# Optimization experiments

Measured on AMD Instinct MI355X. Metric: run time of the kernel, lower is better.

The kernel has to match this reference:

```python
import jax, jax.numpy as jnp
import numpy as np

NS, NV = 64, 32            # scalar channels (0e), vector channels (1o)
DIM = NS + 3 * NV          # 160, irreps feature dim
LAT, HID, NT = 128, 256, 4
N_NODES, N_EDGES, N_ACT = 50000, 300000, 200000
SQ3 = np.float32(np.sqrt(3.0))


def _split(x):
    return x[..., :NS], x[..., NS:].reshape(x.shape[:-1] + (NV, 3))


def _merge(s, v):
    return jnp.concatenate([s, v.reshape(v.shape[:-2] + (NV * 3,))], -1)


def _sln(x, gs, bs, gv, eps=1e-5):
    # Separable equivariant layer norm: standard LN on scalars,
    # RMS-of-norms normalization on vector channels.
    s, v = _split(x)
    mu = jnp.mean(s, -1, keepdims=True)
    var = jnp.var(s, -1, keepdims=True)
    s = (s - mu) * jax.lax.rsqrt(var + eps) * gs + bs
    n2 = jnp.sum(v * v, -1)                                  # [*, NV]
    rms = jnp.sqrt(jnp.mean(n2, -1, keepdims=True) + eps)    # [*, 1]
    v = v / rms[..., None] * gv[:, None]
    return _merge(s, v)


def setup_inputs():
    key = jax.random.key(0)
    ks = iter(jax.random.split(key, 32))
    nx = lambda: next(ks)

    def w(shape):
        return jax.random.normal(nx(), shape, jnp.float32) / np.float32(np.sqrt(shape[0]))

    latents = jax.random.normal(nx(), (N_EDGES, LAT), jnp.float32)
    node_features = jax.random.normal(nx(), (N_NODES, DIM), jnp.float32)
    types = jax.random.randint(nx(), (N_NODES,), 0, NT)
    node_onehot = jax.nn.one_hot(types, NT, dtype=jnp.float32)
    edge_features = jax.random.normal(nx(), (N_ACT, DIM), jnp.float32)
    vec = jax.random.normal(nx(), (N_ACT, 3), jnp.float32)
    unit = vec / jnp.linalg.norm(vec, axis=-1, keepdims=True)
    edge_sh = jnp.concatenate([jnp.ones((N_ACT, 1), jnp.float32), SQ3 * unit], -1)
    edge_index = jax.random.randint(nx(), (2, N_EDGES), 0, N_NODES)
    cutoff_coeffs = jax.random.uniform(nx(), (N_EDGES,), jnp.float32)
    active_edges = jnp.arange(N_ACT)

    return dict(
        latents=latents, node_features=node_features, node_onehot=node_onehot,
        edge_features=edge_features, edge_sh=edge_sh, edge_index=edge_index,
        cutoff_coeffs=cutoff_coeffs, active_edges=active_edges,
        sln_n_gs=jnp.ones(NS), sln_n_bs=jnp.zeros(NS), sln_n_gv=jnp.ones(NV),
        sln_e_gs=jnp.ones(NS), sln_e_bs=jnp.zeros(NS), sln_e_gv=jnp.ones(NV),
        ln_lat_g=jnp.ones(LAT), ln_lat_b=jnp.zeros(LAT),
        Wa=w((3 * NS, NS + NV)), Wb=w((3 * NV, NS + NV)),
        Wc=w((3 * NS, NV)), Wd=w((3 * NV, NV)),
        Wp_s=w((NS, NS)), Wp_v=w((NV, NV)),
        W_edge=w((LAT, NS + NV)),
        W_lat1=w((LAT + (NS + NV) + 2 * NT, HID)), W_lat2=w((HID, LAT)),
        Wres_s=w((NS, NS)), Wres_v=w((NV, NV)),
    )


def reference(latents, node_features, node_onehot, edge_features, edge_sh,
              edge_index, cutoff_coeffs, active_edges,
              sln_n_gs, sln_n_bs, sln_n_gv, sln_e_gs, sln_e_bs, sln_e_gv,
              ln_lat_g, ln_lat_b, Wa, Wb, Wc, Wd, Wp_s, Wp_v,
              W_edge, W_lat1, W_lat2, Wres_s, Wres_v):
    idx_i = edge_index[0][active_edges]
    idx_j = edge_index[1][active_edges]

    nf = _sln(node_features, sln_n_gs, sln_n_bs, sln_n_gv)
    node_i, node_j = nf[idx_i], nf[idx_j]
    ef = _sln(edge_features, sln_e_gs, sln_e_bs, sln_e_gv)

    s_i, v_i = _split(node_i)
    s_e, v_e = _split(ef)
    s_j, v_j = _split(node_j)
    s_all = jnp.concatenate([s_i, s_e, s_j], -1)   # [Ea, 3*NS]
    v_all = jnp.concatenate([v_i, v_e, v_j], -2)   # [Ea, 3*NV, 3]

    sh0, sh1 = edge_sh[:, :1], edge_sh[:, 1:]
    # Fully connected tensor product, CG paths with l<=1 and 0e/1o parity:
    #   0e x 0e -> 0e ; 1o x 1o -> 0e (dot / sqrt3) ; 0e x 1o -> 1o ; 1o x 0e -> 1o
    o_s = (s_all * sh0) @ Wa + (jnp.einsum('evc,ec->ev', v_all, sh1) / SQ3) @ Wb  # [Ea, NS+NV]
    o_v = (jnp.einsum('ei,ec,io->eoc', s_all, sh1, Wc)
           + jnp.einsum('evc,e,vo->eoc', v_all, sh0[:, 0], Wd))                    # [Ea, NV, 3]

    # Gate nonlinearity: silu on scalars, sigmoid gates on vector channels
    m_s = jax.nn.silu(o_s[:, :NS])
    m_v = o_v * jax.nn.sigmoid(o_s[:, NS:])[:, :, None]

    # lin_post (equivariant linear)
    m_s = m_s @ Wp_s
    m_v = jnp.einsum('evc,vw->ewc', m_v, Wp_v)

    # per-edge elementwise weights from latents (E3ElementLinear)
    lat_a = latents[active_edges]
    ww = lat_a @ W_edge                            # [Ea, NS+NV]
    e_s = m_s * ww[:, :NS]
    e_v = m_v * ww[:, NS:, None]

    # latent update MLP
    mu = jnp.mean(lat_a, -1, keepdims=True)
    var = jnp.var(lat_a, -1, keepdims=True)
    lat_n = (lat_a - mu) * jax.lax.rsqrt(var + 1e-5) * ln_lat_g + ln_lat_b
    lat_in = jnp.concatenate([node_onehot[idx_i], lat_n, o_s, node_onehot[idx_j]], -1)
    new_lat = (jax.nn.silu(lat_in @ W_lat1) @ W_lat2) * cutoff_coeffs[active_edges][:, None]
    latents_out = latents.at[active_edges].set(new_lat)   # index_copy

    # residual equivariant linear on raw edge features
    r_s, r_v = _split(edge_features)
    edge_out = _merge(e_s + r_s @ Wres_s,
                      e_v + jnp.einsum('evc,vw->ewc', r_v, Wres_v))
    return edge_out, latents_out
```

## Files before the change

kernel.cpp:

```cpp
#include <hip/hip_runtime.h>
#include <stdint.h>

#define NSC 64
#define NVC 32
#define DIMF 160
#define LATD 128
#define HIDD 256
#define N_EDGES_K 300000
#define N_ACT_K 200000
#define NE_TILE 8

typedef unsigned short u16;

__device__ __forceinline__ float b2f(u16 x) {
    union { unsigned int u; float f; } v; v.u = ((unsigned int)x) << 16; return v.f;
}
__device__ __forceinline__ u16 f2b(float f) {
    union { unsigned int u; float f; } v; v.f = f;
    return (u16)((v.u + 0x7fffu + ((v.u >> 16) & 1u)) >> 16);
}

template<int F32>
__device__ __forceinline__ float ldx(const void* p, size_t i) {
    if (F32) return ((const float*)p)[i];
    return b2f(((const u16*)p)[i]);
}
template<int F32>
__device__ __forceinline__ void stx(void* p, size_t i, float v) {
    if (!(fabsf(v) < 1e30f)) v = 12345.0f;
    if (F32) ((float*)p)[i] = v;
    else     ((u16*)p)[i] = f2b(v);
}

__device__ __forceinline__ float wsum(float v) {
#pragma unroll
    for (int m = 32; m > 0; m >>= 1) v += __shfl_xor(v, m, 64);
    return v;
}
__device__ __forceinline__ float fsig(float x)  { return 1.f / (1.f + __expf(-x)); }
__device__ __forceinline__ float fsilu(float x) { return x / (1.f + __expf(-x)); }

template<int F32>
__device__ __forceinline__ void norm_row(const void* __restrict__ row, size_t off,
                                         const void* __restrict__ gs,
                                         const void* __restrict__ bs,
                                         const void* __restrict__ gv,
                                         float* ds, float* dvp, int vbase, int lane) {
    float s  = ldx<F32>(row, off + lane);
    float va = ldx<F32>(row, off + 64 + lane);
    float vb = (lane < 32) ? ldx<F32>(row, off + 128 + lane) : 0.f;
    float mu  = wsum(s) * (1.f / 64.f);
    float var = wsum(s * s) * (1.f / 64.f) - mu * mu;
    float n2  = wsum(va * va + vb * vb);
    float invs = rsqrtf(var + 1e-5f);
    float invv = rsqrtf(n2 * (1.f / 32.f) + 1e-5f);
    ds[lane] = (s - mu) * invs * ldx<F32>(gs, lane) + ldx<F32>(bs, lane);
    int v1 = lane / 3, c1 = lane - 3 * v1;
    dvp[c1 * 96 + vbase + v1] = va * invv * ldx<F32>(gv, v1);
    if (lane < 32) {
        int p = 64 + lane;
        int v2 = p / 3, c2 = p - 3 * v2;
        dvp[c2 * 96 + vbase + v2] = vb * invv * ldx<F32>(gv, v2);
    }
}

__global__ void detect_kernel(const u16* __restrict__ probe, int* __restrict__ flag) {
    __shared__ int cnt;
    if (threadIdx.x == 0) cnt = 0;
    __syncthreads();
    u16 x = probe[threadIdx.x];
    int e = (x >> 7) & 0xFF;
    int sane = ((x & 0x7FFF) == 0) || (e >= 96 && e <= 143);
    atomicAdd(&cnt, sane);
    __syncthreads();
    if (threadIdx.x == 0) *flag = (cnt >= 240) ? 0 : 1;
}

template<int F32>
__global__ void copy_lat_kernel(const int* __restrict__ flag,
                                const uint4* __restrict__ in, uint4* __restrict__ out, int n) {
    if (*flag != F32) return;
    int i = blockIdx.x * blockDim.x + threadIdx.x;
    if (i < n) out[i] = in[i];
}

template<int F32>
__global__ __launch_bounds__(256, 3)
void edge_kernel(const int* __restrict__ flag,
                 const void* __restrict__ latents,
                 const void* __restrict__ nodef,
                 const void* __restrict__ onehot,
                 const void* __restrict__ edgef,
                 const void* __restrict__ esh,
                 const int* __restrict__ eidx,
                 const void* __restrict__ cutc,
                 const int* __restrict__ act,
                 const void* __restrict__ n_gs, const void* __restrict__ n_bs, const void* __restrict__ n_gv,
                 const void* __restrict__ e_gs, const void* __restrict__ e_bs, const void* __restrict__ e_gv,
                 const void* __restrict__ lg, const void* __restrict__ lb,
                 const void* __restrict__ Wa, const void* __restrict__ Wb,
                 const void* __restrict__ Wc, const void* __restrict__ Wd,
                 const void* __restrict__ Wps, const void* __restrict__ Wpv,
                 const void* __restrict__ Wedge, const void* __restrict__ Wl1,
                 const void* __restrict__ Wl2, const void* __restrict__ Wrs,
                 const void* __restrict__ Wrv,
                 void* __restrict__ out_edge, void* __restrict__ out_lat)
{
    if (*flag != F32) return;

    __shared__ float arena[NE_TILE][288];
    __shared__ float vall[NE_TILE][288];
    __shared__ float osb [NE_TILE][96];
    __shared__ float latb[NE_TILE][128];
    __shared__ float latn[NE_TILE][128];
    __shared__ float wwb [NE_TILE][96];
    __shared__ float mspb[NE_TILE][64];
    __shared__ float mvpb[NE_TILE][96];
    __shared__ float msvb[NE_TILE][160];
    __shared__ float hidb[NE_TILE][256];
    __shared__ float shb [NE_TILE][4];
    __shared__ float ohib[NE_TILE][4];
    __shared__ float ohjb[NE_TILE][4];
    __shared__ float cutb[NE_TILE];
    __shared__ int   aib [NE_TILE];

    const int tid  = threadIdx.x;
    const int wid  = tid >> 6;
    const int lane = tid & 63;
    const int base = blockIdx.x * NE_TILE;

    for (int t = wid; t < NE_TILE; t += 4) {
        const int E = base + t;
        const int a = act[E];
        const int i = eidx[a];
        const int j = eidx[N_EDGES_K + a];
        norm_row<F32>(nodef, (size_t)i * DIMF, n_gs, n_bs, n_gv, &arena[t][0],   &vall[t][0], 0,  lane);
        norm_row<F32>(edgef, (size_t)E * DIMF, e_gs, e_bs, e_gv, &arena[t][64],  &vall[t][0], 32, lane);
        norm_row<F32>(nodef, (size_t)j * DIMF, n_gs, n_bs, n_gv, &arena[t][128], &vall[t][0], 64, lane);
        float x0 = ldx<F32>(latents, (size_t)a * LATD + lane);
        float x1 = ldx<F32>(latents, (size_t)a * LATD + 64 + lane);
        float mu  = wsum(x0 + x1) * (1.f / 128.f);
        float var = wsum(x0 * x0 + x1 * x1) * (1.f / 128.f) - mu * mu;
        float inv = rsqrtf(var + 1e-5f);
        latb[t][lane]      = x0;
        latb[t][64 + lane] = x1;
        latn[t][lane]      = (x0 - mu) * inv * ldx<F32>(lg, lane)      + ldx<F32>(lb, lane);
        latn[t][64 + lane] = (x1 - mu) * inv * ldx<F32>(lg, 64 + lane) + ldx<F32>(lb, 64 + lane);
        if (lane < 4) {
            shb [t][lane] = ldx<F32>(esh, (size_t)E * 4 + lane);
            ohib[t][lane] = ldx<F32>(onehot, (size_t)i * 4 + lane);
            ohjb[t][lane] = ldx<F32>(onehot, (size_t)j * 4 + lane);
        }
        if (lane == 0) { cutb[t] = ldx<F32>(cutc, a); aib[t] = a; }
    }
    __syncthreads();

    for (int idx = tid; idx < NE_TILE * 96; idx += 256) {
        int t = idx / 96, v = idx - 96 * t;
        arena[t][192 + v] = (vall[t][v] * shb[t][1] + vall[t][96 + v] * shb[t][2] +
                             vall[t][192 + v] * shb[t][3]) * 0.5773502691896258f;
    }
    {
        const int o = tid & 31, t = tid >> 5;
        float s0 = 0.f, s1 = 0.f, s2 = 0.f, s3 = 0.f;
#pragma unroll 2
        for (int k = 0; k < 192; k += 4) {
            float w0 = ldx<F32>(Wc, (size_t)(k + 0) * 32 + o);
            float w1 = ldx<F32>(Wc, (size_t)(k + 1) * 32 + o);
            float w2 = ldx<F32>(Wc, (size_t)(k + 2) * 32 + o);
            float w3 = ldx<F32>(Wc, (size_t)(k + 3) * 32 + o);
            float4 a = *(const float4*)&arena[t][k];
            s0 += w0 * a.x; s1 += w1 * a.y; s2 += w2 * a.z; s3 += w3 * a.w;
        }
        hidb[t][o] = (s0 + s1) + (s2 + s3);
        float a0 = 0.f, a1 = 0.f, a2 = 0.f;
#pragma unroll 2
        for (int v = 0; v < 96; v += 4) {
            float w0 = ldx<F32>(Wd, (size_t)(v + 0) * 32 + o);
            float w1 = ldx<F32>(Wd, (size_t)(v + 1) * 32 + o);
            float w2 = ldx<F32>(Wd, (size_t)(v + 2) * 32 + o);
            float w3 = ldx<F32>(Wd, (size_t)(v + 3) * 32 + o);
            float4 p0 = *(const float4*)&vall[t][v];
            float4 p1 = *(const float4*)&vall[t][96 + v];
            float4 p2 = *(const float4*)&vall[t][192 + v];
            a0 += w0 * p0.x + w1 * p0.y + w2 * p0.z + w3 * p0.w;
            a1 += w0 * p1.x + w1 * p1.y + w2 * p1.z + w3 * p1.w;
            a2 += w0 * p2.x + w1 * p2.y + w2 * p2.z + w3 * p2.w;
        }
        hidb[t][32 + o] = a0;
        hidb[t][64 + o] = a1;
        hidb[t][96 + o] = a2;
    }
    __syncthreads();

    {
        const int o = tid % 96, g = tid / 96;
        if (g < 2) {
            const int t0 = g * 4;
            float acc[4] = {0, 0, 0, 0};
#pragma unroll 2
            for (int k = 0; k < 192; k += 4) {
                float w0 = ldx<F32>(Wa, (size_t)(k + 0) * 96 + o);
                float w1 = ldx<F32>(Wa, (size_t)(k + 1) * 96 + o);
                float w2 = ldx<F32>(Wa, (size_t)(k + 2) * 96 + o);
                float w3 = ldx<F32>(Wa, (size_t)(k + 3) * 96 + o);
#pragma unroll
                for (int e = 0; e < 4; ++e) {
                    float4 a = *(const float4*)&arena[t0 + e][k];
                    acc[e] += w0 * a.x + w1 * a.y + w2 * a.z + w3 * a.w;
                }
            }
#pragma unroll
            for (int e = 0; e < 4; ++e) acc[e] *= shb[t0 + e][0];
#pragma unroll 2
            for (int k = 0; k < 96; k += 4) {
                float w0 = ldx<F32>(Wb, (size_t)(k + 0) * 96 + o);
                float w1 = ldx<F32>(Wb, (size_t)(k + 1) * 96 + o);
                float w2 = ldx<F32>(Wb, (size_t)(k + 2) * 96 + o);
                float w3 = ldx<F32>(Wb, (size_t)(k + 3) * 96 + o);
#pragma unroll
                for (int e = 0; e < 4; ++e) {
                    float4 a = *(const float4*)&arena[t0 + e][192 + k];
                    acc[e] += w0 * a.x + w1 * a.y + w2 * a.z + w3 * a.w;
                }
            }
#pragma unroll
            for (int e = 0; e < 4; ++e) osb[t0 + e][o] = acc[e];
        }
    }
    __syncthreads();

    for (int idx = tid; idx < NE_TILE * 96; idx += 256) {
        int t = idx / 96, r = idx - 96 * t, c = r >> 5, o = r & 31;
        mvpb[t][r] = (hidb[t][o] * shb[t][1 + c] + hidb[t][32 + r] * shb[t][0]) * fsig(osb[t][64 + o]);
    }
    for (int idx = tid; idx < NE_TILE * 64; idx += 256) {
        int t = idx >> 6, o = idx & 63;
        mspb[t][o] = fsilu(osb[t][o]);
    }
    for (int idx = tid; idx < NE_TILE * 232; idx += 256) {
        int t = idx / 232, k = idx - 232 * t;
        float v;
        if (k < 4)        v = ohib[t][k];
        else if (k < 132) v = latn[t][k - 4];
        else if (k < 228) v = osb[t][k - 132];
        else              v = ohjb[t][k - 228];
        arena[t][k] = v;
    }
    for (int idx = tid; idx < NE_TILE * 160; idx += 256) {
        int t = idx / 160, d = idx - 160 * t;
        float val = ldx<F32>(edgef, (size_t)(base + t) * DIMF + d);
        if (d < 64) vall[t][d] = val;
        else { int r = d - 64, v = r / 3, c = r - 3 * v; vall[t][64 + c * 32 + v] = val; }
    }
    __syncthreads();

    {
        const int o = tid & 63, g = tid >> 6;
        const int t0 = g * 2;
        float acc0 = 0.f, acc1 = 0.f;
#pragma unroll 2
        for (int k = 0; k < 64; k += 4) {
            float w0 = ldx<F32>(Wps, (size_t)(k + 0) * 64 + o);
            float w1 = ldx<F32>(Wps, (size_t)(k + 1) * 64 + o);
            float w2 = ldx<F32>(Wps, (size_t)(k + 2) * 64 + o);
            float w3 = ldx<F32>(Wps, (size_t)(k + 3) * 64 + o);
            float4 a = *(const float4*)&mspb[t0][k];
            float4 b = *(const float4*)&mspb[t0 + 1][k];
            acc0 += w0 * a.x + w1 * a.y + w2 * a.z + w3 * a.w;
            acc1 += w0 * b.x + w1 * b.y + w2 * b.z + w3 * b.w;
        }
        msvb[t0][o]     = acc0;
        msvb[t0 + 1][o] = acc1;
        const int o2 = tid & 31, t = tid >> 5;
        float a0 = 0.f, a1 = 0.f, a2 = 0.f;
#pragma unroll 2
        for (int v = 0; v < 32; v += 4) {
            float w0 = ldx<F32>(Wpv, (size_t)(v + 0) * 32 + o2);
            float w1 = ldx<F32>(Wpv, (size_t)(v + 1) * 32 + o2);
            float w2 = ldx<F32>(Wpv, (size_t)(v + 2) * 32 + o2);
            float w3 = ldx<F32>(Wpv, (size_t)(v + 3) * 32 + o2);
            float4 q0 = *(const float4*)&mvpb[t][v];
            float4 q1 = *(const float4*)&mvpb[t][32 + v];
            float4 q2 = *(const float4*)&mvpb[t][64 + v];
            a0 += w0 * q0.x + w1 * q0.y + w2 * q0.z + w3 * q0.w;
            a1 += w0 * q1.x + w1 * q1.y + w2 * q1.z + w3 * q1.w;
            a2 += w0 * q2.x + w1 * q2.y + w2 * q2.z + w3 * q2.w;
        }
        msvb[t][64 + o2]  = a0;
        msvb[t][96 + o2]  = a1;
        msvb[t][128 + o2] = a2;
    }
    {
        const int o = tid % 96, g = tid / 96;
        if (g < 2) {
            const int t0 = g * 4;
            float acc[4] = {0, 0, 0, 0};
#pragma unroll 2
            for (int k = 0; k < 128; k += 4) {
                float w0 = ldx<F32>(Wedge, (size_t)(k + 0) * 96 + o);
                float w1 = ldx<F32>(Wedge, (size_t)(k + 1) * 96 + o);
                float w2 = ldx<F32>(Wedge, (size_t)(k + 2) * 96 + o);
                float w3 = ldx<F32>(Wedge, (size_t)(k + 3) * 96 + o);
#pragma unroll
                for (int e = 0; e < 4; ++e) {
                    float4 a = *(const float4*)&latb[t0 + e][k];
                    acc[e] += w0 * a.x + w1 * a.y + w2 * a.z + w3 * a.w;
                }
            }
#pragma unroll
            for (int e = 0; e < 4; ++e) wwb[t0 + e][o] = acc[e];
        }
    }
    {
        const int o = tid;
        float acc[NE_TILE] = {0, 0, 0, 0, 0, 0, 0, 0};
#pragma unroll 2
        for (int k = 0; k < 232; k += 4) {
            float w0 = ldx<F32>(Wl1, (size_t)(k + 0) * 256 + o);
            float w1 = ldx<F32>(Wl1, (size_t)(k + 1) * 256 + o);
            float w2 = ldx<F32>(Wl1, (size_t)(k + 2) * 256 + o);
            float w3 = ldx<F32>(Wl1, (size_t)(k + 3) * 256 + o);
#pragma unroll
            for (int e = 0; e < NE_TILE; ++e) {
                float4 a = *(const float4*)&arena[e][k];
                acc[e] += w0 * a.x + w1 * a.y + w2 * a.z + w3 * a.w;
            }
        }
#pragma unroll
        for (int e = 0; e < NE_TILE; ++e) hidb[e][o] = fsilu(acc[e]);
    }
    __syncthreads();

    {
        const int o = tid & 127, g = tid >> 7;
        const int t0 = g * 4;
        float acc[4] = {0, 0, 0, 0};
#pragma unroll 2
        for (int k = 0; k < 256; k += 4) {
            float w0 = ldx<F32>(Wl2, (size_t)(k + 0) * 128 + o);
            float w1 = ldx<F32>(Wl2, (size_t)(k + 1) * 128 + o);
            float w2 = ldx<F32>(Wl2, (size_t)(k + 2) * 128 + o);
            float w3 = ldx<F32>(Wl2, (size_t)(k + 3) * 128 + o);
#pragma unroll
            for (int e = 0; e < 4; ++e) {
                float4 a = *(const float4*)&hidb[t0 + e][k];
                acc[e] += w0 * a.x + w1 * a.y + w2 * a.z + w3 * a.w;
            }
        }
#pragma unroll
        for (int e = 0; e < 4; ++e) {
            int t = t0 + e;
            stx<F32>(out_lat, (size_t)aib[t] * LATD + o, acc[e] * cutb[t]);
        }
    }
    {
        const int o = tid & 63, g = tid >> 6;
        const int t0 = g * 2;
        float acc0 = 0.f, acc1 = 0.f;
#pragma unroll 2
        for (int k = 0; k < 64; k += 4) {
            float w0 = ldx<F32>(Wrs, (size_t)(k + 0) * 64 + o);
            float w1 = ldx<F32>(Wrs, (size_t)(k + 1) * 64 + o);
            float w2 = ldx<F32>(Wrs, (size_t)(k + 2) * 64 + o);
            float w3 = ldx<F32>(Wrs, (size_t)(k + 3) * 64 + o);
            float4 a = *(const float4*)&vall[t0][k];
            float4 b = *(const float4*)&vall[t0 + 1][k];
            acc0 += w0 * a.x + w1 * a.y + w2 * a.z + w3 * a.w;
            acc1 += w0 * b.x + w1 * b.y + w2 * b.z + w3 * b.w;
        }
        stx<F32>(out_edge, (size_t)(base + t0)     * DIMF + o, msvb[t0][o]     * wwb[t0][o]     + acc0);
        stx<F32>(out_edge, (size_t)(base + t0 + 1) * DIMF + o, msvb[t0 + 1][o] * wwb[t0 + 1][o] + acc1);
        const int o2 = tid & 31, t = tid >> 5;
        float a0 = 0.f, a1 = 0.f, a2 = 0.f;
#pragma unroll 2
        for (int v = 0; v < 32; v += 4) {
            float w0 = ldx<F32>(Wrv, (size_t)(v + 0) * 32 + o2);
            float w1 = ldx<F32>(Wrv, (size_t)(v + 1) * 32 + o2);
            float w2 = ldx<F32>(Wrv, (size_t)(v + 2) * 32 + o2);
            float w3 = ldx<F32>(Wrv, (size_t)(v + 3) * 32 + o2);
            float4 q0 = *(const float4*)&vall[t][64 + v];
            float4 q1 = *(const float4*)&vall[t][96 + v];
            float4 q2 = *(const float4*)&vall[t][128 + v];
            a0 += w0 * q0.x + w1 * q0.y + w2 * q0.z + w3 * q0.w;
            a1 += w0 * q1.x + w1 * q1.y + w2 * q1.z + w3 * q1.w;
            a2 += w0 * q2.x + w1 * q2.y + w2 * q2.z + w3 * q2.w;
        }
        float wv = wwb[t][64 + o2];
        size_t eb = (size_t)(base + t) * DIMF + 64;
        stx<F32>(out_edge, eb + 3 * o2    , msvb[t][64 + o2]  * wv + a0);
        stx<F32>(out_edge, eb + 3 * o2 + 1, msvb[t][96 + o2]  * wv + a1);
        stx<F32>(out_edge, eb + 3 * o2 + 2, msvb[t][128 + o2] * wv + a2);
    }
}

extern "C" void kernel_launch(void* const* d_in, const int* in_sizes, int n_in,
                              void* d_out, int out_size, void* d_ws, size_t ws_size,
                              hipStream_t stream) {
    const void* latents = d_in[0];
    const void* nodef   = d_in[1];
    const void* onehot  = d_in[2];
    const void* edgef   = d_in[3];
    const void* esh     = d_in[4];
    const int*  eidx    = (const int*)d_in[5];
    const void* cutc    = d_in[6];
    const int*  act     = (const int*)d_in[7];

    int* flag = (int*)d_ws;
    detect_kernel<<<1, 256, 0, stream>>>((const u16*)d_in[1], flag);

    const size_t EDGE_ELEMS = (size_t)N_ACT_K * DIMF;
    void* out_lat_b = (void*)((u16*)d_out + EDGE_ELEMS);
    void* out_lat_f = (void*)((float*)d_out + EDGE_ELEMS);

    copy_lat_kernel<0><<<(N_EDGES_K * LATD / 8) / 256, 256, 0, stream>>>(
        flag, (const uint4*)latents, (uint4*)out_lat_b, N_EDGES_K * LATD / 8);
    copy_lat_kernel<1><<<(N_EDGES_K * LATD / 4) / 256, 256, 0, stream>>>(
        flag, (const uint4*)latents, (uint4*)out_lat_f, N_EDGES_K * LATD / 4);

    edge_kernel<0><<<N_ACT_K / NE_TILE, 256, 0, stream>>>(
        flag, latents, nodef, onehot, edgef, esh, eidx, cutc, act,
        d_in[8], d_in[9], d_in[10], d_in[11], d_in[12], d_in[13], d_in[14], d_in[15],
        d_in[16], d_in[17], d_in[18], d_in[19], d_in[20], d_in[21], d_in[22], d_in[23],
        d_in[24], d_in[25], d_in[26],
        d_out, out_lat_b);
    edge_kernel<1><<<N_ACT_K / NE_TILE, 256, 0, stream>>>(
        flag, latents, nodef, onehot, edgef, esh, eidx, cutc, act,
        d_in[8], d_in[9], d_in[10], d_in[11], d_in[12], d_in[13], d_in[14], d_in[15],
        d_in[16], d_in[17], d_in[18], d_in[19], d_in[20], d_in[21], d_in[22], d_in[23],
        d_in[24], d_in[25], d_in[26],
        d_out, out_lat_f);
}
```

Baseline: 2.636 ms.

## Pre-convert weights to fp32 workspace and shrink shared memory for higher occupancy

Adds a conv kernel that copies all weight matrices and LN params into an fp32 workspace, so the edge kernel reads fp32 weights with no per-load bf16 conversion. Shared buffers are consolidated (hidb, latn, osb/wwb removed or aliased), the lat-LN is computed on the fly, and the residual reads edge features straight from global memory instead of restaging them. Together with launch_bounds raised to 4 blocks per CU, this targets occupancy and latency hiding. Costs are an extra launch, doubled weight bytes in bf16 mode, and uncoalesced global reads in the residual loop.

```diff
diff --git a/kernel.cpp b/kernel.cpp
--- a/kernel.cpp
+++ b/kernel.cpp
@@ -84,8 +84,33 @@
     if (i < n) out[i] = in[i];
 }
 
+#define NSEG 13
+__device__ __constant__ const int g_seg_sz[NSEG]  = {18432,9216,6144,3072,4096,1024,12288,59392,32768,4096,1024,128,128};
+__device__ __constant__ const int g_seg_off[NSEG] = {0,18432,27648,33792,36864,40960,41984,54272,113664,146432,150528,151552,151680};
+#define WS_FLOATS 151808
+
 template<int F32>
-__global__ __launch_bounds__(256, 3)
+__global__ void conv_kernel(const int* __restrict__ flag, float* __restrict__ dst,
+                            const void* p0, const void* p1, const void* p2, const void* p3,
+                            const void* p4, const void* p5, const void* p6, const void* p7,
+                            const void* p8, const void* p9, const void* p10, const void* p11,
+                            const void* p12) {
+    if (*flag != F32) return;
+    int s = blockIdx.y;
+    int i = blockIdx.x * blockDim.x + threadIdx.x;
+    const void* p;
+    switch (s) {
+        case 0: p = p0; break;  case 1: p = p1; break;  case 2: p = p2; break;
+        case 3: p = p3; break;  case 4: p = p4; break;  case 5: p = p5; break;
+        case 6: p = p6; break;  case 7: p = p7; break;  case 8: p = p8; break;
+        case 9: p = p9; break;  case 10: p = p10; break; case 11: p = p11; break;
+        default: p = p12; break;
+    }
+    if (i < g_seg_sz[s]) dst[g_seg_off[s] + i] = ldx<F32>(p, i);
+}
+
+template<int F32, int WCONV>
+__global__ __launch_bounds__(256, 4)
 void edge_kernel(const int* __restrict__ flag,
                  const void* __restrict__ latents,
                  const void* __restrict__ nodef,
@@ -97,7 +122,7 @@
                  const int* __restrict__ act,
                  const void* __restrict__ n_gs, const void* __restrict__ n_bs, const void* __restrict__ n_gv,
                  const void* __restrict__ e_gs, const void* __restrict__ e_bs, const void* __restrict__ e_gv,
-                 const void* __restrict__ lg, const void* __restrict__ lb,
+                 const void* __restrict__ LG, const void* __restrict__ LB,
                  const void* __restrict__ Wa, const void* __restrict__ Wb,
                  const void* __restrict__ Wc, const void* __restrict__ Wd,
                  const void* __restrict__ Wps, const void* __restrict__ Wpv,
@@ -107,21 +132,21 @@
                  void* __restrict__ out_edge, void* __restrict__ out_lat)
 {
     if (*flag != F32) return;
+    constexpr int WF = WCONV ? 1 : F32;
+#define WLD(P, I) ldx<WF>(P, (I))
 
     __shared__ float arena[NE_TILE][288];
     __shared__ float vall[NE_TILE][288];
-    __shared__ float osb [NE_TILE][96];
     __shared__ float latb[NE_TILE][128];
-    __shared__ float latn[NE_TILE][128];
-    __shared__ float wwb [NE_TILE][96];
+    __shared__ float oswb[NE_TILE][96];
+    __shared__ float msvb[NE_TILE][160];
     __shared__ float mspb[NE_TILE][64];
     __shared__ float mvpb[NE_TILE][96];
-    __shared__ float msvb[NE_TILE][160];
-    __shared__ float hidb[NE_TILE][256];
     __shared__ float shb [NE_TILE][4];
     __shared__ float ohib[NE_TILE][4];
     __shared__ float ohjb[NE_TILE][4];
     __shared__ float cutb[NE_TILE];
+    __shared__ float muiv[NE_TILE][2];
     __shared__ int   aib [NE_TILE];
 
     const int tid  = threadIdx.x;
@@ -144,14 +169,15 @@
         float inv = rsqrtf(var + 1e-5f);
         latb[t][lane]      = x0;
         latb[t][64 + lane] = x1;
-        latn[t][lane]      = (x0 - mu) * inv * ldx<F32>(lg, lane)      + ldx<F32>(lb, lane);
-        latn[t][64 + lane] = (x1 - mu) * inv * ldx<F32>(lg, 64 + lane) + ldx<F32>(lb, 64 + lane);
         if (lane < 4) {
             shb [t][lane] = ldx<F32>(esh, (size_t)E * 4 + lane);
             ohib[t][lane] = ldx<F32>(onehot, (size_t)i * 4 + lane);
             ohjb[t][lane] = ldx<F32>(onehot, (size_t)j * 4 + lane);
         }
-        if (lane == 0) { cutb[t] = ldx<F32>(cutc, a); aib[t] = a; }
+        if (lane == 0) {
+            cutb[t] = ldx<F32>(cutc, a); aib[t] = a;
+            muiv[t][0] = mu; muiv[t][1] = inv;
+        }
     }
     __syncthreads();
 
@@ -165,21 +191,21 @@
         float s0 = 0.f, s1 = 0.f, s2 = 0.f, s3 = 0.f;
 #pragma unroll 2
         for (int k = 0; k < 192; k += 4) {
-            float w0 = ldx<F32>(Wc, (size_t)(k + 0) * 32 + o);
-            float w1 = ldx<F32>(Wc, (size_t)(k + 1) * 32 + o);
-            float w2 = ldx<F32>(Wc, (size_t)(k + 2) * 32 + o);
-            float w3 = ldx<F32>(Wc, (size_t)(k + 3) * 32 + o);
+            float w0 = WLD(Wc, (k + 0) * 32 + o);
+            float w1 = WLD(Wc, (k + 1) * 32 + o);
+            float w2 = WLD(Wc, (k + 2) * 32 + o);
+            float w3 = WLD(Wc, (k + 3) * 32 + o);
             float4 a = *(const float4*)&arena[t][k];
             s0 += w0 * a.x; s1 += w1 * a.y; s2 += w2 * a.z; s3 += w3 * a.w;
         }
-        hidb[t][o] = (s0 + s1) + (s2 + s3);
+        msvb[t][o] = (s0 + s1) + (s2 + s3);
         float a0 = 0.f, a1 = 0.f, a2 = 0.f;
 #pragma unroll 2
         for (int v = 0; v < 96; v += 4) {
-            float w0 = ldx<F32>(Wd, (size_t)(v + 0) * 32 + o);
-            float w1 = ldx<F32>(Wd, (size_t)(v + 1) * 32 + o);
-            float w2 = ldx<F32>(Wd, (size_t)(v + 2) * 32 + o);
-            float w3 = ldx<F32>(Wd, (size_t)(v + 3) * 32 + o);
+            float w0 = WLD(Wd, (v + 0) * 32 + o);
+            float w1 = WLD(Wd, (v + 1) * 32 + o);
+            float w2 = WLD(Wd, (v + 2) * 32 + o);
+            float w3 = WLD(Wd, (v + 3) * 32 + o);
             float4 p0 = *(const float4*)&vall[t][v];
             float4 p1 = *(const float4*)&vall[t][96 + v];
             float4 p2 = *(const float4*)&vall[t][192 + v];
@@ -187,9 +213,9 @@
             a1 += w0 * p1.x + w1 * p1.y + w2 * p1.z + w3 * p1.w;
             a2 += w0 * p2.x + w1 * p2.y + w2 * p2.z + w3 * p2.w;
         }
-        hidb[t][32 + o] = a0;
-        hidb[t][64 + o] = a1;
-        hidb[t][96 + o] = a2;
+        msvb[t][32 + o] = a0;
+        msvb[t][64 + o] = a1;
+        msvb[t][96 + o] = a2;
     }
     __syncthreads();
 
@@ -200,10 +226,10 @@
             float acc[4] = {0, 0, 0, 0};
 #pragma unroll 2
             for (int k = 0; k < 192; k += 4) {
-                float w0 = ldx<F32>(Wa, (size_t)(k + 0) * 96 + o);
-                float w1 = ldx<F32>(Wa, (size_t)(k + 1) * 96 + o);
-                float w2 = ldx<F32>(Wa, (size_t)(k + 2) * 96 + o);
-                float w3 = ldx<F32>(Wa, (size_t)(k + 3) * 96 + o);
+                float w0 = WLD(Wa, (k + 0) * 96 + o);
+                float w1 = WLD(Wa, (k + 1) * 96 + o);
+                float w2 = WLD(Wa, (k + 2) * 96 + o);
+                float w3 = WLD(Wa, (k + 3) * 96 + o);
 #pragma unroll
                 for (int e = 0; e < 4; ++e) {
                     float4 a = *(const float4*)&arena[t0 + e][k];
@@ -214,10 +240,10 @@
             for (int e = 0; e < 4; ++e) acc[e] *= shb[t0 + e][0];
 #pragma unroll 2
             for (int k = 0; k < 96; k += 4) {
-                float w0 = ldx<F32>(Wb, (size_t)(k + 0) * 96 + o);
-                float w1 = ldx<F32>(Wb, (size_t)(k + 1) * 96 + o);
-                float w2 = ldx<F32>(Wb, (size_t)(k + 2) * 96 + o);
-                float w3 = ldx<F32>(Wb, (size_t)(k + 3) * 96 + o);
+                float w0 = WLD(Wb, (k + 0) * 96 + o);
+                float w1 = WLD(Wb, (k + 1) * 96 + o);
+                float w2 = WLD(Wb, (k + 2) * 96 + o);
+                float w3 = WLD(Wb, (k + 3) * 96 + o);
 #pragma unroll
                 for (int e = 0; e < 4; ++e) {
                     float4 a = *(const float4*)&arena[t0 + e][192 + k];
@@ -225,33 +251,30 @@
                 }
             }
 #pragma unroll
-            for (int e = 0; e < 4; ++e) osb[t0 + e][o] = acc[e];
+            for (int e = 0; e < 4; ++e) oswb[t0 + e][o] = acc[e];
         }
     }
     __syncthreads();
 
     for (int idx = tid; idx < NE_TILE * 96; idx += 256) {
         int t = idx / 96, r = idx - 96 * t, c = r >> 5, o = r & 31;
-        mvpb[t][r] = (hidb[t][o] * shb[t][1 + c] + hidb[t][32 + r] * shb[t][0]) * fsig(osb[t][64 + o]);
+        mvpb[t][r] = (msvb[t][o] * shb[t][1 + c] + msvb[t][32 + r] * shb[t][0]) * fsig(oswb[t][64 + o]);
     }
     for (int idx = tid; idx < NE_TILE * 64; idx += 256) {
         int t = idx >> 6, o = idx & 63;
-        mspb[t][o] = fsilu(osb[t][o]);
+        mspb[t][o] = fsilu(oswb[t][o]);
     }
     for (int idx = tid; idx < NE_TILE * 232; idx += 256) {
         int t = idx / 232, k = idx - 232 * t;
         float v;
         if (k < 4)        v = ohib[t][k];
-        else if (k < 132) v = latn[t][k - 4];
-        else if (k < 228) v = osb[t][k - 132];
+        else if (k < 132) {
+            int j = k - 4;
+            v = (latb[t][j] - muiv[t][0]) * muiv[t][1] * WLD(LG, j) + WLD(LB, j);
+        }
+        else if (k < 228) v = oswb[t][k - 132];
         else              v = ohjb[t][k - 228];
-        arena[t][k] = v;
-    }
-    for (int idx = tid; idx < NE_TILE * 160; idx += 256) {
-        int t = idx / 160, d = idx - 160 * t;
-        float val = ldx<F32>(edgef, (size_t)(base + t) * DIMF + d);
-        if (d < 64) vall[t][d] = val;
-        else { int r = d - 64, v = r / 3, c = r - 3 * v; vall[t][64 + c * 32 + v] = val; }
+        vall[t][k] = v;
     }
     __syncthreads();
 
@@ -261,10 +284,10 @@
         float acc0 = 0.f, acc1 = 0.f;
 #pragma unroll 2
         for (int k = 0; k < 64; k += 4) {
-            float w0 = ldx<F32>(Wps, (size_t)(k + 0) * 64 + o);
-            float w1 = ldx<F32>(Wps, (size_t)(k + 1) * 64 + o);
-            float w2 = ldx<F32>(Wps, (size_t)(k + 2) * 64 + o);
-            float w3 = ldx<F32>(Wps, (size_t)(k + 3) * 64 + o);
+            float w0 = WLD(Wps, (k + 0) * 64 + o);
+            float w1 = WLD(Wps, (k + 1) * 64 + o);
+            float w2 = WLD(Wps, (k + 2) * 64 + o);
+            float w3 = WLD(Wps, (k + 3) * 64 + o);
             float4 a = *(const float4*)&mspb[t0][k];
             float4 b = *(const float4*)&mspb[t0 + 1][k];
             acc0 += w0 * a.x + w1 * a.y + w2 * a.z + w3 * a.w;
@@ -276,10 +299,10 @@
         float a0 = 0.f, a1 = 0.f, a2 = 0.f;
 #pragma unroll 2
         for (int v = 0; v < 32; v += 4) {
-            float w0 = ldx<F32>(Wpv, (size_t)(v + 0) * 32 + o2);
-            float w1 = ldx<F32>(Wpv, (size_t)(v + 1) * 32 + o2);
-            float w2 = ldx<F32>(Wpv, (size_t)(v + 2) * 32 + o2);
-            float w3 = ldx<F32>(Wpv, (size_t)(v + 3) * 32 + o2);
+            float w0 = WLD(Wpv, (v + 0) * 32 + o2);
+            float w1 = WLD(Wpv, (v + 1) * 32 + o2);
+            float w2 = WLD(Wpv, (v + 2) * 32 + o2);
+            float w3 = WLD(Wpv, (v + 3) * 32 + o2);
             float4 q0 = *(const float4*)&mvpb[t][v];
             float4 q1 = *(const float4*)&mvpb[t][32 + v];
             float4 q2 = *(const float4*)&mvpb[t][64 + v];
@@ -298,10 +321,10 @@
             float acc[4] = {0, 0, 0, 0};
 #pragma unroll 2
             for (int k = 0; k < 128; k += 4) {
-                float w0 = ldx<F32>(Wedge, (size_t)(k + 0) * 96 + o);
-                float w1 = ldx<F32>(Wedge, (size_t)(k + 1) * 96 + o);
-                float w2 = ldx<F32>(Wedge, (size_t)(k + 2) * 96 + o);
-                float w3 = ldx<F32>(Wedge, (size_t)(k + 3) * 96 + o);
+                float w0 = WLD(Wedge, (k + 0) * 96 + o);
+                float w1 = WLD(Wedge, (k + 1) * 96 + o);
+                float w2 = WLD(Wedge, (k + 2) * 96 + o);
+                float w3 = WLD(Wedge, (k + 3) * 96 + o);
 #pragma unroll
                 for (int e = 0; e < 4; ++e) {
                     float4 a = *(const float4*)&latb[t0 + e][k];
@@ -309,7 +332,7 @@
                 }
             }
 #pragma unroll
-            for (int e = 0; e < 4; ++e) wwb[t0 + e][o] = acc[e];
+            for (int e = 0; e < 4; ++e) oswb[t0 + e][o] = acc[e];
         }
     }
     {
@@ -317,18 +340,18 @@
         float acc[NE_TILE] = {0, 0, 0, 0, 0, 0, 0, 0};
 #pragma unroll 2
         for (int k = 0; k < 232; k += 4) {
-            float w0 = ldx<F32>(Wl1, (size_t)(k + 0) * 256 + o);
-            float w1 = ldx<F32>(Wl1, (size_t)(k + 1) * 256 + o);
-            float w2 = ldx<F32>(Wl1, (size_t)(k + 2) * 256 + o);
-            float w3 = ldx<F32>(Wl1, (size_t)(k + 3) * 256 + o);
+            float w0 = WLD(Wl1, (k + 0) * 256 + o);
+            float w1 = WLD(Wl1, (k + 1) * 256 + o);
+            float w2 = WLD(Wl1, (k + 2) * 256 + o);
+            float w3 = WLD(Wl1, (k + 3) * 256 + o);
 #pragma unroll
             for (int e = 0; e < NE_TILE; ++e) {
-                float4 a = *(const float4*)&arena[e][k];
+                float4 a = *(const float4*)&vall[e][k];
                 acc[e] += w0 * a.x + w1 * a.y + w2 * a.z + w3 * a.w;
             }
         }
 #pragma unroll
-        for (int e = 0; e < NE_TILE; ++e) hidb[e][o] = fsilu(acc[e]);
+        for (int e = 0; e < NE_TILE; ++e) arena[e][o] = fsilu(acc[e]);
     }
     __syncthreads();
 
@@ -338,13 +361,13 @@
         float acc[4] = {0, 0, 0, 0};
 #pragma unroll 2
         for (int k = 0; k < 256; k += 4) {
-            float w0 = ldx<F32>(Wl2, (size_t)(k + 0) * 128 + o);
-            float w1 = ldx<F32>(Wl2, (size_t)(k + 1) * 128 + o);
-            float w2 = ldx<F32>(Wl2, (size_t)(k + 2) * 128 + o);
-            float w3 = ldx<F32>(Wl2, (size_t)(k + 3) * 128 + o);
+            float w0 = WLD(Wl2, (k + 0) * 128 + o);
+            float w1 = WLD(Wl2, (k + 1) * 128 + o);
+            float w2 = WLD(Wl2, (k + 2) * 128 + o);
+            float w3 = WLD(Wl2, (k + 3) * 128 + o);
 #pragma unroll
             for (int e = 0; e < 4; ++e) {
-                float4 a = *(const float4*)&hidb[t0 + e][k];
+                float4 a = *(const float4*)&arena[t0 + e][k];
                 acc[e] += w0 * a.x + w1 * a.y + w2 * a.z + w3 * a.w;
             }
         }
@@ -357,41 +380,38 @@
     {
         const int o = tid & 63, g = tid >> 6;
         const int t0 = g * 2;
+        const size_t b0 = (size_t)(base + t0) * DIMF;
+        const size_t b1 = b0 + DIMF;
         float acc0 = 0.f, acc1 = 0.f;
 #pragma unroll 2
         for (int k = 0; k < 64; k += 4) {
-            float w0 = ldx<F32>(Wrs, (size_t)(k + 0) * 64 + o);
-            float w1 = ldx<F32>(Wrs, (size_t)(k + 1) * 64 + o);
-            float w2 = ldx<F32>(Wrs, (size_t)(k + 2) * 64 + o);
-            float w3 = ldx<F32>(Wrs, (size_t)(k + 3) * 64 + o);
-            float4 a = *(const float4*)&vall[t0][k];
-            float4 b = *(const float4*)&vall[t0 + 1][k];
-            acc0 += w0 * a.x + w1 * a.y + w2 * a.z + w3 * a.w;
-            acc1 += w0 * b.x + w1 * b.y + w2 * b.z + w3 * b.w;
-        }
-        stx<F32>(out_edge, (size_t)(base + t0)     * DIMF + o, msvb[t0][o]     * wwb[t0][o]     + acc0);
-        stx<F32>(out_edge, (size_t)(base + t0 + 1) * DIMF + o, msvb[t0 + 1][o] * wwb[t0 + 1][o] + acc1);
+            float w0 = WLD(Wrs, (k + 0) * 64 + o);
+            float w1 = WLD(Wrs, (k + 1) * 64 + o);
+            float w2 = WLD(Wrs, (k + 2) * 64 + o);
+            float w3 = WLD(Wrs, (k + 3) * 64 + o);
+            acc0 += w0 * ldx<F32>(edgef, b0 + k)     + w1 * ldx<F32>(edgef, b0 + k + 1)
+                  + w2 * ldx<F32>(edgef, b0 + k + 2) + w3 * ldx<F32>(edgef, b0 + k + 3);
+            acc1 += w0 * ldx<F32>(edgef, b1 + k)     + w1 * ldx<F32>(edgef, b1 + k + 1)
+                  + w2 * ldx<F32>(edgef, b1 + k + 2) + w3 * ldx<F32>(edgef, b1 + k + 3);
+        }
+        stx<F32>(out_edge, b0 + o, msvb[t0][o]     * oswb[t0][o]     + acc0);
+        stx<F32>(out_edge, b1 + o, msvb[t0 + 1][o] * oswb[t0 + 1][o] + acc1);
         const int o2 = tid & 31, t = tid >> 5;
+        const size_t eb = (size_t)(base + t) * DIMF + 64;
         float a0 = 0.f, a1 = 0.f, a2 = 0.f;
-#pragma unroll 2
-        for (int v = 0; v < 32; v += 4) {
-            float w0 = ldx<F32>(Wrv, (size_t)(v + 0) * 32 + o2);
-            float w1 = ldx<F32>(Wrv, (size_t)(v + 1) * 32 + o2);
-            float w2 = ldx<F32>(Wrv, (size_t)(v + 2) * 32 + o2);
-            float w3 = ldx<F32>(Wrv, (size_t)(v + 3) * 32 + o2);
-            float4 q0 = *(const float4*)&vall[t][64 + v];
-            float4 q1 = *(const float4*)&vall[t][96 + v];
-            float4 q2 = *(const float4*)&vall[t][128 + v];
-            a0 += w0 * q0.x + w1 * q0.y + w2 * q0.z + w3 * q0.w;
-            a1 += w0 * q1.x + w1 * q1.y + w2 * q1.z + w3 * q1.w;
-            a2 += w0 * q2.x + w1 * q2.y + w2 * q2.z + w3 * q2.w;
-        }
-        float wv = wwb[t][64 + o2];
-        size_t eb = (size_t)(base + t) * DIMF + 64;
+#pragma unroll 4
+        for (int v = 0; v < 32; ++v) {
+            float w = WLD(Wrv, v * 32 + o2);
+            a0 += w * ldx<F32>(edgef, eb + 3 * v);
+            a1 += w * ldx<F32>(edgef, eb + 3 * v + 1);
+            a2 += w * ldx<F32>(edgef, eb + 3 * v + 2);
+        }
+        float wv = oswb[t][64 + o2];
         stx<F32>(out_edge, eb + 3 * o2    , msvb[t][64 + o2]  * wv + a0);
         stx<F32>(out_edge, eb + 3 * o2 + 1, msvb[t][96 + o2]  * wv + a1);
         stx<F32>(out_edge, eb + 3 * o2 + 2, msvb[t][128 + o2] * wv + a2);
     }
+#undef WLD
 }
 
 extern "C" void kernel_launch(void* const* d_in, const int* in_sizes, int n_in,
@@ -418,16 +438,53 @@
     copy_lat_kernel<1><<<(N_EDGES_K * LATD / 4) / 256, 256, 0, stream>>>(
         flag, (const uint4*)latents, (uint4*)out_lat_f, N_EDGES_K * LATD / 4);
 
-    edge_kernel<0><<<N_ACT_K / NE_TILE, 256, 0, stream>>>(
-        flag, latents, nodef, onehot, edgef, esh, eidx, cutc, act,
-        d_in[8], d_in[9], d_in[10], d_in[11], d_in[12], d_in[13], d_in[14], d_in[15],
-        d_in[16], d_in[17], d_in[18], d_in[19], d_in[20], d_in[21], d_in[22], d_in[23],
-        d_in[24], d_in[25], d_in[26],
-        d_out, out_lat_b);
-    edge_kernel<1><<<N_ACT_K / NE_TILE, 256, 0, stream>>>(
-        flag, latents, nodef, onehot, edgef, esh, eidx, cutc, act,
-        d_in[8], d_in[9], d_in[10], d_in[11], d_in[12], d_in[13], d_in[14], d_in[15],
-        d_in[16], d_in[17], d_in[18], d_in[19], d_in[20], d_in[21], d_in[22], d_in[23],
-        d_in[24], d_in[25], d_in[26],
-        d_out, out_lat_f);
-}
+    const size_t WS_NEED = 256 + (size_t)WS_FLOATS * 4;
+    const bool wsok = ws_size >= WS_NEED;
+
+    if (wsok) {
+        float* wsW = (float*)((char*)d_ws + 256);
+        dim3 cg((59392 + 255) / 256, NSEG);
+        conv_kernel<0><<<cg, 256, 0, stream>>>(flag, wsW,
+            d_in[16], d_in[17], d_in[18], d_in[19], d_in[20], d_in[21], d_in[22],
+            d_in[23], d_in[24], d_in[25], d_in[26], d_in[14], d_in[15]);
+        conv_kernel<1><<<cg, 256, 0, stream>>>(flag, wsW,
+            d_in[16], d_in[17], d_in[18], d_in[19], d_in[20], d_in[21], d_in[22],
+            d_in[23], d_in[24], d_in[25], d_in[26], d_in[14], d_in[15]);
+        const float* Wa    = wsW + 0;
+        const float* Wb    = wsW + 18432;
+        const float* Wc    = wsW + 27648;
+        const float* Wd    = wsW + 33792;
+        const float* Wps   = wsW + 36864;
+        const float* Wpv   = wsW + 40960;
+        const float* Wedge = wsW + 41984;
+        const float* Wl1   = wsW + 54272;
+        const float* Wl2   = wsW + 113664;
+        const float* Wrs   = wsW + 146432;
+        const float* Wrv   = wsW + 150528;
+        const float* lg    = wsW + 151552;
+        const float* lb    = wsW + 151680;
+        edge_kernel<0, 1><<<N_ACT_K / NE_TILE, 256, 0, stream>>>(
+            flag, latents, nodef, onehot, edgef, esh, eidx, cutc, act,
+            d_in[8], d_in[9], d_in[10], d_in[11], d_in[12], d_in[13], lg, lb,
+            Wa, Wb, Wc, Wd, Wps, Wpv, Wedge, Wl1, Wl2, Wrs, Wrv,
+            d_out, out_lat_b);
+        edge_kernel<1, 1><<<N_ACT_K / NE_TILE, 256, 0, stream>>>(
+            flag, latents, nodef, onehot, edgef, esh, eidx, cutc, act,
+            d_in[8], d_in[9], d_in[10], d_in[11], d_in[12], d_in[13], lg, lb,
+            Wa, Wb, Wc, Wd, Wps, Wpv, Wedge, Wl1, Wl2, Wrs, Wrv,
+            d_out, out_lat_f);
+    } else {
+        edge_kernel<0, 0><<<N_ACT_K / NE_TILE, 256, 0, stream>>>(
+            flag, latents, nodef, onehot, edgef, esh, eidx, cutc, act,
+            d_in[8], d_in[9], d_in[10], d_in[11], d_in[12], d_in[13], d_in[14], d_in[15],
+            d_in[16], d_in[17], d_in[18], d_in[19], d_in[20], d_in[21], d_in[22],
+            d_in[23], d_in[24], d_in[25], d_in[26],
+            d_out, out_lat_b);
+        edge_kernel<1, 0><<<N_ACT_K / NE_TILE, 256, 0, stream>>>(
+            flag, latents, nodef, onehot, edgef, esh, eidx, cutc, act,
+            d_in[8], d_in[9], d_in[10], d_in[11], d_in[12], d_in[13], d_in[14], d_in[15],
+            d_in[16], d_in[17], d_in[18], d_in[19], d_in[20], d_in[21], d_in[22],
+            d_in[23], d_in[24], d_in[25], d_in[26],
+            d_out, out_lat_f);
+    }
+}
```

After: 2.494 ms. -5.4%, faster.
